# Optimization experiments

Measured on AMD Instinct MI355X. Metric: run time of the kernel, lower is better.

The kernel has to match this reference:

```python
import jax, jax.numpy as jnp
import numpy as np

N_NODES = 100000   # vertices
N_HEDGES = 20000   # hyperedges
NNZ = 1600000      # incidence entries (avg vertex degree 16)
IN_FT = 128
OUT_FT = 128


def setup_inputs() -> dict:
    key = jax.random.key(0)
    ks = jax.random.split(key, 8)
    stdv = 1.0 / np.sqrt(OUT_FT)
    x = jax.random.normal(ks[0], (N_NODES, IN_FT), dtype=jnp.float32)
    weight = jax.random.uniform(ks[1], (IN_FT, OUT_FT), dtype=jnp.float32, minval=-stdv, maxval=stdv)
    bias = jax.random.uniform(ks[2], (OUT_FT,), dtype=jnp.float32, minval=-stdv, maxval=stdv)
    node_idx = jax.random.randint(ks[3], (NNZ,), 0, N_NODES, dtype=jnp.int32)
    edge_idx = jax.random.randint(ks[4], (NNZ,), 0, N_HEDGES, dtype=jnp.int32)
    h_val = jnp.ones((NNZ,), dtype=jnp.float32)
    dv_inv = jax.random.uniform(ks[5], (N_NODES,), dtype=jnp.float32, minval=0.01, maxval=1.0)
    de_inv = jax.random.uniform(ks[6], (N_HEDGES,), dtype=jnp.float32, minval=0.01, maxval=1.0)
    return {"x": x, "weight": weight, "bias": bias, "node_idx": node_idx,
            "edge_idx": edge_idx, "h_val": h_val, "dv_inv": dv_inv, "de_inv": de_inv}


def reference(x, weight, bias, node_idx, edge_idx, h_val, dv_inv, de_inv):
    # dense map: X W + b
    x_mapped = jnp.matmul(x, weight) + bias                      # [N, F]
    # vertex-side degree scaling
    x_norm = x_mapped * dv_inv[:, None]                          # [N, F]
    # E = H^T x_norm : scatter vertex rows into hyperedges (spmm with COO H)
    msgs = x_norm[node_idx] * h_val[:, None]                     # [nnz, F]
    E = jax.ops.segment_sum(msgs, edge_idx, num_segments=N_HEDGES)  # [M, F]
    # hyperedge-side degree scaling
    E2 = E * de_inv[:, None]                                     # [M, F]
    # F_out = H E2 : scatter hyperedge rows back to vertices
    msgs2 = E2[edge_idx] * h_val[:, None]                        # [nnz, F]
    F_out = jax.ops.segment_sum(msgs2, node_idx, num_segments=N_NODES)  # [N, F]
    y = F_out * dv_inv[:, None]
    return y + x_mapped
```

## Files before the change

### kernel.cpp

```cpp
#include <hip/hip_runtime.h>


#define F 128
#define NBE 128
#define NBN 64
#define M_E 20000
#define RB_N 25000
#define R_N 4

__device__ __forceinline__ unsigned short f2bf(float f) {
    unsigned u = __float_as_uint(f);
    unsigned r = (u + 0x7FFF + ((u >> 16) & 1)) >> 16;
    return (unsigned short)r;
}
__device__ __forceinline__ float bf2f(unsigned short h) {
    return __uint_as_float((unsigned)h << 16);
}

__global__ __launch_bounds__(512) void kA_e(const int* __restrict__ ei,
                                            int* __restrict__ part2, int nnz) {
    __shared__ int sh[M_E];
    int b = blockIdx.x, t = threadIdx.x;
    for (int k = t; k < M_E; k += 512) sh[k] = 0;
    __syncthreads();
    int ch = (nnz + NBE - 1) / NBE;
    int i0 = b * ch, i1 = i0 + ch < nnz ? i0 + ch : nnz;
    for (int i = i0 + t; i < i1; i += 512) atomicAdd(&sh[ei[i]], 1);
    __syncthreads();
    for (int k = t; k < M_E; k += 512) part2[(size_t)b * M_E + k] = sh[k];
}

__global__ __launch_bounds__(512) void kA_n(const int* __restrict__ ni,
                                            int* __restrict__ partN2, int nnz) {
    __shared__ int sh[RB_N];
    int b = blockIdx.x >> 2, r = blockIdx.x & 3, t = threadIdx.x;
    for (int k = t; k < RB_N; k += 512) sh[k] = 0;
    __syncthreads();
    int ch = (nnz + NBN - 1) / NBN;
    int i0 = b * ch, i1 = i0 + ch < nnz ? i0 + ch : nnz;
    int lo = r * RB_N;
    for (int i = i0 + t; i < i1; i += 512) {
        int lb = ni[i] - lo;
        if ((unsigned)lb < (unsigned)RB_N) atomicAdd(&sh[lb], 1);
    }
    __syncthreads();
    for (int k = t; k < RB_N; k += 512)
        partN2[((size_t)(r * NBN + b)) * RB_N + k] = sh[k];
}

__global__ void kB(int* __restrict__ part2, int* __restrict__ cnt, int bins, int nb) {
    int bin = blockIdx.x * blockDim.x + threadIdx.x;
    if (bin >= bins) return;
    int run = 0;
#pragma unroll 8
    for (int b = 0; b < nb; ++b) {
        size_t idx = (size_t)b * bins + bin;
        int v = part2[idx];
        part2[idx] = run;
        run += v;
    }
    cnt[bin] = run;
}

__global__ void k_scan1(const int* __restrict__ cnt, int* __restrict__ excl,
                        int* __restrict__ part, int n) {
    __shared__ int s[256];
    int t = threadIdx.x;
    int base = blockIdx.x * 1024 + t * 4;
    int v0 = (base + 0 < n) ? cnt[base + 0] : 0;
    int v1 = (base + 1 < n) ? cnt[base + 1] : 0;
    int v2 = (base + 2 < n) ? cnt[base + 2] : 0;
    int v3 = (base + 3 < n) ? cnt[base + 3] : 0;
    s[t] = v0 + v1 + v2 + v3;
    __syncthreads();
    for (int off = 1; off < 256; off <<= 1) {
        int add = (t >= off) ? s[t - off] : 0;
        __syncthreads();
        s[t] += add;
        __syncthreads();
    }
    int r = (t > 0) ? s[t - 1] : 0;
    if (base + 0 < n) excl[base + 0] = r; r += v0;
    if (base + 1 < n) excl[base + 1] = r; r += v1;
    if (base + 2 < n) excl[base + 2] = r; r += v2;
    if (base + 3 < n) excl[base + 3] = r;
    if (t == 255) part[blockIdx.x] = s[255];
}

__global__ void k_scan2(int* __restrict__ part, int n) {
    __shared__ int s[256];
    int t = threadIdx.x;
    s[t] = (t < n) ? part[t] : 0;
    __syncthreads();
    for (int off = 1; off < 256; off <<= 1) {
        int add = (t >= off) ? s[t - off] : 0;
        __syncthreads();
        s[t] += add;
        __syncthreads();
    }
    if (t < n) part[t] = (t > 0) ? s[t - 1] : 0;
}

__global__ void k_scan3(int* __restrict__ start, const int* __restrict__ part, int n) {
    int i = blockIdx.x * blockDim.x + threadIdx.x;
    if (i < n) start[i] += part[i >> 10];
}

__global__ __launch_bounds__(512) void kC_e(const int* __restrict__ ei, const int* __restrict__ ni,
                                            const float* __restrict__ hv, const float* __restrict__ dv,
                                            const int* __restrict__ start, const int* __restrict__ part2,
                                            int2* __restrict__ eslot, int nnz) {
    __shared__ int sh[M_E];
    int b = blockIdx.x, t = threadIdx.x;
    for (int k = t; k < M_E; k += 512)
        sh[k] = start[k] + part2[(size_t)b * M_E + k];
    __syncthreads();
    int ch = (nnz + NBE - 1) / NBE;
    int i0 = b * ch, i1 = i0 + ch < nnz ? i0 + ch : nnz;
    for (int i = i0 + t; i < i1; i += 512) {
        int e = ei[i], nd = ni[i];
        float v = hv[i] * dv[nd];
        int p = atomicAdd(&sh[e], 1);
        eslot[p] = make_int2(nd, __float_as_int(v));
    }
}

__global__ __launch_bounds__(512) void kC_n(const int* __restrict__ ei, const int* __restrict__ ni,
                                            const float* __restrict__ hv,
                                            const int* __restrict__ start, const int* __restrict__ partN2,
                                            int2* __restrict__ nslot, int nnz) {
    __shared__ int sh[RB_N];
    int b = blockIdx.x >> 2, r = blockIdx.x & 3, t = threadIdx.x;
    int lo = r * RB_N;
    for (int k = t; k < RB_N; k += 512)
        sh[k] = start[lo + k] + partN2[((size_t)(r * NBN + b)) * RB_N + k];
    __syncthreads();
    int ch = (nnz + NBN - 1) / NBN;
    int i0 = b * ch, i1 = i0 + ch < nnz ? i0 + ch : nnz;
    for (int i = i0 + t; i < i1; i += 512) {
        int lb = ni[i] - lo;
        if ((unsigned)lb < (unsigned)RB_N) {
            int e = ei[i];
            float h = hv[i];
            int p = atomicAdd(&sh[lb], 1);
            nslot[p] = make_int2(e, __float_as_int(h));
        }
    }
}

__device__ __forceinline__ float f4_get(const float4& v, int k) {
    return k == 0 ? v.x : k == 1 ? v.y : k == 2 ? v.z : v.w;
}

__global__ __launch_bounds__(256) void k_gemm(const float* __restrict__ x,
                                              const float* __restrict__ w,
                                              const float* __restrict__ bias,
                                              float* __restrict__ y,
                                              unsigned short* __restrict__ xmb, int N) {
    __shared__ float sw[32 * 128];
    __shared__ float sx[128 * 36];
    int t = threadIdx.x;
    int row0 = blockIdx.x * 128;
    int cg = (t & 15) * 8;
    int rg = (t >> 4) * 8;
    float acc[8][8];
#pragma unroll
    for (int a = 0; a < 8; a++)
#pragma unroll
        for (int b = 0; b < 8; b++) acc[a][b] = 0.f;

    const float4* x4 = (const float4*)x;
    const float4* w4 = (const float4*)w;

    for (int kc = 0; kc < 4; ++kc) {
        __syncthreads();
        for (int i = t; i < 1024; i += 256) {
            int k = i >> 5, c4 = i & 31;
            ((float4*)sw)[i] = w4[(kc * 32 + k) * 32 + c4];
        }
        for (int i = t; i < 1024; i += 256) {
            int r = i >> 3, c4 = i & 7;
            float4 vv = make_float4(0.f, 0.f, 0.f, 0.f);
            if (row0 + r < N) vv = x4[(size_t)(row0 + r) * 32 + kc * 8 + c4];
            *(float4*)&sx[r * 36 + c4 * 4] = vv;
        }
        __syncthreads();
#pragma unroll
        for (int k4 = 0; k4 < 8; ++k4) {
            float4 xa[8];
#pragma unroll
            for (int rr = 0; rr < 8; rr++)
                xa[rr] = *(const float4*)&sx[(rg + rr) * 36 + k4 * 4];
#pragma unroll
            for (int kk = 0; kk < 4; kk++) {
                float4 wa0 = *(const float4*)&sw[(k4 * 4 + kk) * 128 + cg];
                float4 wa1 = *(const float4*)&sw[(k4 * 4 + kk) * 128 + cg + 4];
#pragma unroll
                for (int rr = 0; rr < 8; rr++) {
                    float xv = f4_get(xa[rr], kk);
                    acc[rr][0] += xv * wa0.x; acc[rr][1] += xv * wa0.y;
                    acc[rr][2] += xv * wa0.z; acc[rr][3] += xv * wa0.w;
                    acc[rr][4] += xv * wa1.x; acc[rr][5] += xv * wa1.y;
                    acc[rr][6] += xv * wa1.z; acc[rr][7] += xv * wa1.w;
                }
            }
        }
    }

    float4 b0 = *(const float4*)&bias[cg];
    float4 b1 = *(const float4*)&bias[cg + 4];
#pragma unroll
    for (int rr = 0; rr < 8; rr++) {
        int r = row0 + rg + rr;
        if (r < N) {
            float o[8] = {acc[rr][0] + b0.x, acc[rr][1] + b0.y,
                          acc[rr][2] + b0.z, acc[rr][3] + b0.w,
                          acc[rr][4] + b1.x, acc[rr][5] + b1.y,
                          acc[rr][6] + b1.z, acc[rr][7] + b1.w};
            *(float4*)&y[(size_t)r * F + cg]     = make_float4(o[0], o[1], o[2], o[3]);
            *(float4*)&y[(size_t)r * F + cg + 4] = make_float4(o[4], o[5], o[6], o[7]);
            ushort4 h0 = {f2bf(o[0]), f2bf(o[1]), f2bf(o[2]), f2bf(o[3])};
            ushort4 h1 = {f2bf(o[4]), f2bf(o[5]), f2bf(o[6]), f2bf(o[7])};
            *(ushort4*)&xmb[(size_t)r * F + cg]     = h0;
            *(ushort4*)&xmb[(size_t)r * F + cg + 4] = h1;
        }
    }
}

__global__ __launch_bounds__(256) void k_edge(const unsigned short* __restrict__ xmb,
                                              const int2* __restrict__ slot,
                                              const float* __restrict__ de,
                                              const int* __restrict__ start,
                                              const int* __restrict__ cnt,
                                              unsigned short* __restrict__ E2b, int M) {
    int wid = blockIdx.x * 4 + (threadIdx.x >> 6);
    if (wid >= M) return;
    int lane = threadIdx.x & 63;
    int hl = lane >> 5;
    int l  = lane & 31;
    int p = start[wid], c = cnt[wid];
    float a0 = 0.f, a1 = 0.f, a2 = 0.f, a3 = 0.f;
    int j = hl;
    for (; j + 2 < c; j += 4) {
        int2 s0 = slot[p + j];
        int2 s1 = slot[p + j + 2];
        float c0 = __int_as_float(s0.y), c1 = __int_as_float(s1.y);
        ushort4 v0 = *(const ushort4*)(xmb + (size_t)s0.x * F + l * 4);
        ushort4 v1 = *(const ushort4*)(xmb + (size_t)s1.x * F + l * 4);
        a0 += c0 * bf2f(v0.x) + c1 * bf2f(v1.x);
        a1 += c0 * bf2f(v0.y) + c1 * bf2f(v1.y);
        a2 += c0 * bf2f(v0.z) + c1 * bf2f(v1.z);
        a3 += c0 * bf2f(v0.w) + c1 * bf2f(v1.w);
    }
    if (j < c) {
        int2 s0 = slot[p + j];
        float c0 = __int_as_float(s0.y);
        ushort4 v0 = *(const ushort4*)(xmb + (size_t)s0.x * F + l * 4);
        a0 += c0 * bf2f(v0.x); a1 += c0 * bf2f(v0.y);
        a2 += c0 * bf2f(v0.z); a3 += c0 * bf2f(v0.w);
    }
    a0 += __shfl_xor(a0, 32);
    a1 += __shfl_xor(a1, 32);
    a2 += __shfl_xor(a2, 32);
    a3 += __shfl_xor(a3, 32);
    if (hl == 0) {
        float s = de[wid];
        ushort4 o = {f2bf(a0 * s), f2bf(a1 * s), f2bf(a2 * s), f2bf(a3 * s)};
        *(ushort4*)(E2b + (size_t)wid * F + l * 4) = o;
    }
}

__global__ __launch_bounds__(256) void k_node(const unsigned short* __restrict__ E2b,
                                              const int2* __restrict__ slot,
                                              const float* __restrict__ dv,
                                              const int* __restrict__ start,
                                              const int* __restrict__ cnt,
                                              float* out, int N) {
    int wid = blockIdx.x * 4 + (threadIdx.x >> 6);
    if (wid >= N) return;
    int lane = threadIdx.x & 63;
    int hl = lane >> 5;
    int l  = lane & 31;
    int p = start[wid], c = cnt[wid];
    float a0 = 0.f, a1 = 0.f, a2 = 0.f, a3 = 0.f;
    int j = hl;
    for (; j + 2 < c; j += 4) {
        int2 s0 = slot[p + j];
        int2 s1 = slot[p + j + 2];
        float c0 = __int_as_float(s0.y), c1 = __int_as_float(s1.y);
        ushort4 v0 = *(const ushort4*)(E2b + (size_t)s0.x * F + l * 4);
        ushort4 v1 = *(const ushort4*)(E2b + (size_t)s1.x * F + l * 4);
        a0 += c0 * bf2f(v0.x) + c1 * bf2f(v1.x);
        a1 += c0 * bf2f(v0.y) + c1 * bf2f(v1.y);
        a2 += c0 * bf2f(v0.z) + c1 * bf2f(v1.z);
        a3 += c0 * bf2f(v0.w) + c1 * bf2f(v1.w);
    }
    if (j < c) {
        int2 s0 = slot[p + j];
        float c0 = __int_as_float(s0.y);
        ushort4 v0 = *(const ushort4*)(E2b + (size_t)s0.x * F + l * 4);
        a0 += c0 * bf2f(v0.x); a1 += c0 * bf2f(v0.y);
        a2 += c0 * bf2f(v0.z); a3 += c0 * bf2f(v0.w);
    }
    a0 += __shfl_xor(a0, 32);
    a1 += __shfl_xor(a1, 32);
    a2 += __shfl_xor(a2, 32);
    a3 += __shfl_xor(a3, 32);
    if (hl == 0) {
        float dvn = dv[wid];
        float4 xv = *(const float4*)(out + (size_t)wid * F + l * 4);
        *(float4*)(out + (size_t)wid * F + l * 4) =
            make_float4(a0 * dvn + xv.x, a1 * dvn + xv.y,
                        a2 * dvn + xv.z, a3 * dvn + xv.w);
    }
}

extern "C" void kernel_launch(void* const* d_in, const int* in_sizes, int n_in,
                              void* d_out, int out_size, void* d_ws, size_t ws_size,
                              hipStream_t stream) {
    const float* x      = (const float*)d_in[0];
    const float* w      = (const float*)d_in[1];
    const float* bias   = (const float*)d_in[2];
    const int*   ni     = (const int*)d_in[3];
    const int*   ei     = (const int*)d_in[4];
    const float* hv     = (const float*)d_in[5];
    const float* dv     = (const float*)d_in[6];
    const float* de     = (const float*)d_in[7];
    float* out = (float*)d_out;

    const int N   = in_sizes[0] / F;
    const int NNZ = in_sizes[3];
    const int M   = in_sizes[7];

    int* wsp        = (int*)d_ws;
    int* edge_cnt   = wsp;
    int* node_cnt   = edge_cnt + M;
    int* edge_start = node_cnt + N;
    int* node_start = edge_start + M;
    int* partE      = node_start + N;
    int* partN      = partE + 256;
    int* partE2     = partN + 256;
    int* partN2     = partE2 + (size_t)NBE * M_E;
    int2* eslot     = (int2*)(partN2 + (size_t)R_N * NBN * RB_N);
    int2* nslot     = eslot + NNZ;
    unsigned short* xmb = (unsigned short*)partN2;
    unsigned short* E2b = (unsigned short*)partE2;

    const int gScanE = (M + 1023) / 1024;
    const int gScanN = (N + 1023) / 1024;

    kA_e<<<NBE, 512, 0, stream>>>(ei, partE2, NNZ);
    kA_n<<<NBN * R_N, 512, 0, stream>>>(ni, partN2, NNZ);

    kB<<<(M + 255) / 256, 256, 0, stream>>>(partE2, edge_cnt, M, NBE);
    for (int r = 0; r < R_N; ++r)
        kB<<<(RB_N + 255) / 256, 256, 0, stream>>>(partN2 + (size_t)r * NBN * RB_N,
                                                   node_cnt + (size_t)r * RB_N, RB_N, NBN);

    k_scan1<<<gScanE, 256, 0, stream>>>(edge_cnt, edge_start, partE, M);
    k_scan1<<<gScanN, 256, 0, stream>>>(node_cnt, node_start, partN, N);
    k_scan2<<<1, 256, 0, stream>>>(partE, gScanE);
    k_scan2<<<1, 256, 0, stream>>>(partN, gScanN);
    k_scan3<<<(M + 255) / 256, 256, 0, stream>>>(edge_start, partE, M);
    k_scan3<<<(N + 255) / 256, 256, 0, stream>>>(node_start, partN, N);

    kC_e<<<NBE, 512, 0, stream>>>(ei, ni, hv, dv, edge_start, partE2, eslot, NNZ);
    kC_n<<<NBN * R_N, 512, 0, stream>>>(ei, ni, hv, node_start, partN2, nslot, NNZ);

    k_gemm<<<(N + 127) / 128, 256, 0, stream>>>(x, w, bias, out, xmb, N);

    k_edge<<<(M + 3) / 4, 256, 0, stream>>>(xmb, eslot, de, edge_start, edge_cnt, E2b, M);
    k_node<<<(N + 3) / 4, 256, 0, stream>>>(E2b, nslot, dv, node_start, node_cnt, out, N);
}
```

Baseline: 523.8 us.

## Replace FP32 SIMT GEMM with bf16 MFMA using pre-transposed bf16 weights

Rewrites the dense X·W+b kernel to use 16x16x32 bf16 MFMA instructions. A new small kernel transposes the weights and converts them to bf16. The GEMM loads x rows straight from global memory and converts them to bf16 in registers, with no shared-memory staging. This cuts the cost of the FP32 FMA GEMM, but lowers the input precision of the dense map to bf16. The output stores are now scattered scalar writes rather than vectorized float4 writes.

```diff
diff --git a/kernel.cpp b/kernel.cpp
--- a/kernel.cpp
+++ b/kernel.cpp
@@ -7,6 +7,9 @@
 #define M_E 20000
 #define RB_N 25000
 #define R_N 4
+
+typedef __attribute__((ext_vector_type(8))) short bf16x8;
+typedef __attribute__((ext_vector_type(4))) float f32x4;
 
 __device__ __forceinline__ unsigned short f2bf(float f) {
     unsigned u = __float_as_uint(f);
@@ -148,81 +151,72 @@
     }
 }
 
-__device__ __forceinline__ float f4_get(const float4& v, int k) {
-    return k == 0 ? v.x : k == 1 ? v.y : k == 2 ? v.z : v.w;
+__global__ __launch_bounds__(256) void k_wt(const float* __restrict__ w,
+                                            unsigned short* __restrict__ wt) {
+    int i = blockIdx.x * 256 + threadIdx.x;
+    int n = i >> 7, k = i & 127;
+    wt[(size_t)n * F + k] = f2bf(w[(size_t)k * F + n]);
 }
 
 __global__ __launch_bounds__(256) void k_gemm(const float* __restrict__ x,
-                                              const float* __restrict__ w,
+                                              const unsigned short* __restrict__ wt,
                                               const float* __restrict__ bias,
                                               float* __restrict__ y,
                                               unsigned short* __restrict__ xmb, int N) {
-    __shared__ float sw[32 * 128];
-    __shared__ float sx[128 * 36];
     int t = threadIdx.x;
-    int row0 = blockIdx.x * 128;
-    int cg = (t & 15) * 8;
-    int rg = (t >> 4) * 8;
-    float acc[8][8];
-#pragma unroll
-    for (int a = 0; a < 8; a++)
-#pragma unroll
-        for (int b = 0; b < 8; b++) acc[a][b] = 0.f;
-
-    const float4* x4 = (const float4*)x;
-    const float4* w4 = (const float4*)w;
-
-    for (int kc = 0; kc < 4; ++kc) {
-        __syncthreads();
-        for (int i = t; i < 1024; i += 256) {
-            int k = i >> 5, c4 = i & 31;
-            ((float4*)sw)[i] = w4[(kc * 32 + k) * 32 + c4];
+    int wv = t >> 6, lane = t & 63;
+    int lrow = lane & 15, kg = lane >> 4;
+    int row0 = blockIdx.x * 128 + wv * 32;
+
+    f32x4 acc[2][8];
+#pragma unroll
+    for (int rf = 0; rf < 2; ++rf)
+#pragma unroll
+        for (int cf = 0; cf < 8; ++cf) acc[rf][cf] = (f32x4){0.f, 0.f, 0.f, 0.f};
+
+#pragma unroll
+    for (int ks = 0; ks < 4; ++ks) {
+        bf16x8 a[2];
+#pragma unroll
+        for (int rf = 0; rf < 2; ++rf) {
+            int r = row0 + rf * 16 + lrow;
+            float4 q0 = make_float4(0.f, 0.f, 0.f, 0.f);
+            float4 q1 = make_float4(0.f, 0.f, 0.f, 0.f);
+            if (r < N) {
+                const float* xp = x + (size_t)r * F + ks * 32 + kg * 8;
+                q0 = *(const float4*)xp;
+                q1 = *(const float4*)(xp + 4);
+            }
+            bf16x8 av;
+            av[0] = (short)f2bf(q0.x); av[1] = (short)f2bf(q0.y);
+            av[2] = (short)f2bf(q0.z); av[3] = (short)f2bf(q0.w);
+            av[4] = (short)f2bf(q1.x); av[5] = (short)f2bf(q1.y);
+            av[6] = (short)f2bf(q1.z); av[7] = (short)f2bf(q1.w);
+            a[rf] = av;
         }
-        for (int i = t; i < 1024; i += 256) {
-            int r = i >> 3, c4 = i & 7;
-            float4 vv = make_float4(0.f, 0.f, 0.f, 0.f);
-            if (row0 + r < N) vv = x4[(size_t)(row0 + r) * 32 + kc * 8 + c4];
-            *(float4*)&sx[r * 36 + c4 * 4] = vv;
+#pragma unroll
+        for (int cf = 0; cf < 8; ++cf) {
+            bf16x8 b = *(const bf16x8*)(wt + ((size_t)(cf * 16 + lrow)) * F + ks * 32 + kg * 8);
+            acc[0][cf] = __builtin_amdgcn_mfma_f32_16x16x32_bf16(a[0], b, acc[0][cf], 0, 0, 0);
+            acc[1][cf] = __builtin_amdgcn_mfma_f32_16x16x32_bf16(a[1], b, acc[1][cf], 0, 0, 0);
         }
-        __syncthreads();
-#pragma unroll
-        for (int k4 = 0; k4 < 8; ++k4) {
-            float4 xa[8];
-#pragma unroll
-            for (int rr = 0; rr < 8; rr++)
-                xa[rr] = *(const float4*)&sx[(rg + rr) * 36 + k4 * 4];
-#pragma unroll
-            for (int kk = 0; kk < 4; kk++) {
-                float4 wa0 = *(const float4*)&sw[(k4 * 4 + kk) * 128 + cg];
-                float4 wa1 = *(const float4*)&sw[(k4 * 4 + kk) * 128 + cg + 4];
-#pragma unroll
-                for (int rr = 0; rr < 8; rr++) {
-                    float xv = f4_get(xa[rr], kk);
-                    acc[rr][0] += xv * wa0.x; acc[rr][1] += xv * wa0.y;
-                    acc[rr][2] += xv * wa0.z; acc[rr][3] += xv * wa0.w;
-                    acc[rr][4] += xv * wa1.x; acc[rr][5] += xv * wa1.y;
-                    acc[rr][6] += xv * wa1.z; acc[rr][7] += xv * wa1.w;
+    }
+
+#pragma unroll
+    for (int cf = 0; cf < 8; ++cf) {
+        int c = cf * 16 + lrow;
+        float bb = bias[c];
+#pragma unroll
+        for (int rf = 0; rf < 2; ++rf) {
+#pragma unroll
+            for (int j = 0; j < 4; ++j) {
+                int r = row0 + rf * 16 + kg * 4 + j;
+                if (r < N) {
+                    float o = acc[rf][cf][j] + bb;
+                    y[(size_t)r * F + c] = o;
+                    xmb[(size_t)r * F + c] = f2bf(o);
                 }
             }
-        }
-    }
-
-    float4 b0 = *(const float4*)&bias[cg];
-    float4 b1 = *(const float4*)&bias[cg + 4];
-#pragma unroll
-    for (int rr = 0; rr < 8; rr++) {
-        int r = row0 + rg + rr;
-        if (r < N) {
-            float o[8] = {acc[rr][0] + b0.x, acc[rr][1] + b0.y,
-                          acc[rr][2] + b0.z, acc[rr][3] + b0.w,
-                          acc[rr][4] + b1.x, acc[rr][5] + b1.y,
-                          acc[rr][6] + b1.z, acc[rr][7] + b1.w};
-            *(float4*)&y[(size_t)r * F + cg]     = make_float4(o[0], o[1], o[2], o[3]);
-            *(float4*)&y[(size_t)r * F + cg + 4] = make_float4(o[4], o[5], o[6], o[7]);
-            ushort4 h0 = {f2bf(o[0]), f2bf(o[1]), f2bf(o[2]), f2bf(o[3])};
-            ushort4 h1 = {f2bf(o[4]), f2bf(o[5]), f2bf(o[6]), f2bf(o[7])};
-            *(ushort4*)&xmb[(size_t)r * F + cg]     = h0;
-            *(ushort4*)&xmb[(size_t)r * F + cg + 4] = h1;
         }
     }
 }
@@ -343,11 +337,14 @@
     int* partN2     = partE2 + (size_t)NBE * M_E;
     int2* eslot     = (int2*)(partN2 + (size_t)R_N * NBN * RB_N);
     int2* nslot     = eslot + NNZ;
+    unsigned short* wtb = (unsigned short*)(nslot + NNZ);
     unsigned short* xmb = (unsigned short*)partN2;
     unsigned short* E2b = (unsigned short*)partE2;
 
     const int gScanE = (M + 1023) / 1024;
     const int gScanN = (N + 1023) / 1024;
+
+    k_wt<<<64, 256, 0, stream>>>(w, wtb);
 
     kA_e<<<NBE, 512, 0, stream>>>(ei, partE2, NNZ);
     kA_n<<<NBN * R_N, 512, 0, stream>>>(ni, partN2, NNZ);
@@ -367,7 +364,7 @@
     kC_e<<<NBE, 512, 0, stream>>>(ei, ni, hv, dv, edge_start, partE2, eslot, NNZ);
     kC_n<<<NBN * R_N, 512, 0, stream>>>(ei, ni, hv, node_start, partN2, nslot, NNZ);
 
-    k_gemm<<<(N + 127) / 128, 256, 0, stream>>>(x, w, bias, out, xmb, N);
+    k_gemm<<<(N + 127) / 128, 256, 0, stream>>>(x, wtb, bias, out, xmb, N);
 
     k_edge<<<(M + 3) / 4, 256, 0, stream>>>(xmb, eslot, de, edge_start, edge_cnt, E2b, M);
     k_node<<<(N + 3) / 4, 256, 0, stream>>>(E2b, nslot, dv, node_start, node_cnt, out, N);
```

New measurement: 515.4 us. No clear change (-1.6%).
